# Kernel tuning notes

Measured on AMD Instinct MI355X. Metric: run time of the kernel, lower is better.

## Reference

```python
import jax, jax.numpy as jnp
import numpy as np

TEMP = 1.0
EULER_GAMMA = 0.5772156649015329
BIG = 1.0e9


def setup_inputs() -> dict:
    key = jax.random.key(0)
    k = jax.random.split(key, 8)
    B, N, D, H = 32, 1024, 1024, 512  # batch, seq, d_model, hidden_size//2
    queries = jax.random.normal(k[0], (B, N, D), jnp.float32)
    queries_mask = jnp.ones((B, N), dtype=bool)
    W1 = jax.random.normal(k[1], (D, H), jnp.float32) * 0.02
    b1 = jnp.zeros((H,), jnp.float32)
    W2 = jax.random.normal(k[2], (H, 1), jnp.float32) * 0.02
    b2 = jnp.zeros((1,), jnp.float32)
    uniform_noise = jax.random.uniform(k[3], (B, N, 1), jnp.float32, 0.0, 1e-5)
    gumbel_noise = jax.random.gumbel(k[4], (B, N, 1), jnp.float32)
    return {"queries": queries, "queries_mask": queries_mask, "W1": W1, "b1": b1,
            "W2": W2, "b2": b2, "uniform_noise": uniform_noise,
            "gumbel_noise": gumbel_noise, "action_refinement": 1}


def reference(queries, queries_mask, W1, b1, W2, b2, uniform_noise, gumbel_noise, action_refinement):
    B, N, D = queries.shape
    # block0: Dense(H, relu) -> Dense(1); then softplus clamp + log + tiny uniform noise
    h = jax.nn.relu(jnp.einsum('bnd,dh->bnh', queries, W1) + b1)
    acts = jnp.einsum('bnh,ho->bno', h, W2) + b2                      # [B,N,1]
    acts = jnp.log(jnp.maximum(jax.nn.softplus(acts), 1e-5)) + uniform_noise
    acts = jnp.repeat(acts, action_refinement, axis=0)                # [BR,N,1]
    vmask = jnp.repeat(queries_mask[:, None, :].astype(jnp.float32), action_refinement, axis=0)  # [BR,1,N]
    n_valid = jnp.sum(vmask, axis=-1)                                 # [BR,1]
    mask_n1 = jnp.transpose(vmask, (0, 2, 1))                         # [BR,N,1]
    sqz_mask = mask_n1[..., 0]                                        # [BR,N]
    masked_acts = jnp.where(mask_n1 > 0, acts, -1e6)                  # [BR,N,1]
    perturb = masked_acts + gumbel_noise                              # [BR,N,1]
    # deterministic NeuralSort
    s = (jnp.exp(perturb) * mask_n1)[..., 0]                          # [BR,N]
    A = jnp.abs(s[:, :, None] - s[:, None, :])                        # [BR,N,N]
    Bmat = jnp.sum(A, axis=-1, keepdims=True)                         # A @ (1 1^T): row sums broadcast
    scaling = (N + 1 - 2 * (jnp.arange(N) + 1)).astype(jnp.float32)   # [N]
    C = s[:, :, None] * scaling[None, None, :]                        # [BR,N,N]
    P_hat = jnp.transpose(C - Bmat, (0, 2, 1)) - (1.0 - vmask) * BIG  # [BR,N,N]
    # greedy argmax permutation extraction (find_permu), vectorized over batch
    BR = P_hat.shape[0]
    def step(flag, row):                                              # row: [BR,N]
        tmp = row - flag * BIG
        idx = jnp.argmax(tmp, axis=-1)
        flag = jnp.maximum(flag, jax.nn.one_hot(idx, N, dtype=flag.dtype))
        return flag, idx
    _, idxs = jax.lax.scan(step, jnp.zeros((BR, N), jnp.float32), jnp.transpose(P_hat, (1, 0, 2)))
    chosen = jnp.transpose(idxs).astype(jnp.int32)                    # [BR,N]
    chosen = jnp.concatenate([jnp.zeros((BR, 1), jnp.int32), chosen[:, :-1]], axis=-1)
    id_permu = jnp.arange(N, dtype=jnp.int32)[None, :]
    permu = jnp.where(sqz_mask > 0, chosen, id_permu)                 # [BR,N]
    sample_permu = jax.nn.one_hot(permu, N, axis=-1, dtype=jnp.float32)
    # Plackett-Luce log-likelihood of sampled permutation
    exp_actis = jnp.exp(jnp.take_along_axis(masked_acts[..., 0], permu, axis=-1))
    rev_cumsum = jnp.cumsum(exp_actis[:, ::-1], axis=-1)[:, ::-1]
    eps = 1e-20
    log_nom = (jnp.log(exp_actis + eps) - jnp.log(rev_cumsum + eps)) * sqz_mask
    log_nom = jnp.sum(log_nom, axis=-1, keepdims=True)                # [BR,1]
    log_norm = jnp.zeros_like(log_nom)
    # KL term
    sqz_acts = acts[..., 0]
    kl1 = n_valid * (np.log(TEMP) - 1.0 + EULER_GAMMA * (1.0 / TEMP - 1.0))
    s1 = (1.0 / TEMP) * jnp.sum(sqz_acts * sqz_mask, axis=-1).reshape(-1, 1)
    s2 = jnp.sum(jnp.exp(-1.0 / TEMP * jnp.maximum(sqz_acts * sqz_mask, -20.0 * TEMP)), axis=-1).reshape(-1, 1) - (jnp.float32(N) - n_valid)
    kl = kl1 + s1 + s2 * jnp.exp(jax.lax.lgamma(jnp.float32(1.0 + 1.0 / TEMP)))
    return sample_permu, masked_acts[..., 0], kl, log_nom, log_norm
```

## Files before the change

### kernel.cpp

```cpp
#include <hip/hip_runtime.h>
#include <math.h>

#define BB 32
#define NN 1024
#define DD 1024
#define HH 512

#define OUT0_OFF 0
#define OUT1_OFF (BB * NN * NN)
#define OUT2_OFF (OUT1_OFF + BB * NN)
#define OUT3_OFF (OUT2_OFF + BB)
#define OUT4_OFF (OUT3_OFF + BB)

#define WS_ACTS 0
#define WS_W1T  131072
#define WS_RANK 1179648

typedef __attribute__((ext_vector_type(8))) short short8;
typedef __attribute__((ext_vector_type(4))) float floatx4;
typedef __attribute__((ext_vector_type(4))) unsigned int uintx4;

__device__ inline unsigned int cvtpk(float a, float b) {
    unsigned int r;
    asm("v_cvt_pk_bf16_f32 %0, %1, %2" : "=v"(r) : "v"(a), "v"(b));
    return r;
}

__global__ __launch_bounds__(64) void w1t_kernel(const float* __restrict__ W1,
                                                 unsigned short* __restrict__ Bfrag)
{
    const int s  = blockIdx.x;
    const int tn = blockIdx.y;
    const int l  = threadIdx.x;
    const int c  = l & 15, qd = l >> 4;
    const int n  = tn * 16 + c;
    float v[8];
    #pragma unroll
    for (int e = 0; e < 8; ++e)
        v[e] = W1[(size_t)(s * 32 + qd * 8 + e) * HH + n];
    uintx4 u;
    u.x = cvtpk(v[0], v[1]);
    u.y = cvtpk(v[2], v[3]);
    u.z = cvtpk(v[4], v[5]);
    u.w = cvtpk(v[6], v[7]);
    *(uintx4*)(Bfrag + ((size_t)(s * 32 + tn) * 64 + l) * 8) = u;
}

#define MT 64

__global__ __launch_bounds__(256, 2) void gemm_acts_kernel(
    const float* __restrict__ q, const unsigned short* __restrict__ Bfrag,
    const float* __restrict__ b1, const float* __restrict__ W2,
    const float* __restrict__ b2, const float* __restrict__ unoise,
    float* __restrict__ acts_ws, float* __restrict__ out1)
{
    __shared__ float red[MT][4];

    const int tid  = threadIdx.x;
    const int w    = tid >> 6;
    const int lane = tid & 63;
    const int c    = lane & 15;
    const int qd   = lane >> 4;
    const int m0   = blockIdx.x * MT;

    floatx4 acc[8][4];
    #pragma unroll
    for (int tn = 0; tn < 8; ++tn)
        #pragma unroll
        for (int tm = 0; tm < 4; ++tm)
            acc[tn][tm] = (floatx4){0.f, 0.f, 0.f, 0.f};

    const float* aptr[4];
    #pragma unroll
    for (int tm = 0; tm < 4; ++tm)
        aptr[tm] = q + (size_t)(m0 + tm * 16 + c) * DD + qd * 8;

    const short8* bp = (const short8*)Bfrag;
    const int bbase = w * 8 * 64 + lane;

    #pragma unroll 2
    for (int s = 0; s < 32; ++s) {
        short8 af[4];
        #pragma unroll
        for (int tm = 0; tm < 4; ++tm) {
            float4 v0 = *(const float4*)(aptr[tm] + s * 32);
            float4 v1 = *(const float4*)(aptr[tm] + s * 32 + 4);
            uintx4 u;
            u.x = cvtpk(v0.x, v0.y);
            u.y = cvtpk(v0.z, v0.w);
            u.z = cvtpk(v1.x, v1.y);
            u.w = cvtpk(v1.z, v1.w);
            af[tm] = __builtin_bit_cast(short8, u);
        }
        #pragma unroll
        for (int tn = 0; tn < 8; ++tn) {
            short8 bf = bp[(size_t)s * 32 * 64 + bbase + tn * 64];
            #pragma unroll
            for (int tm = 0; tm < 4; ++tm)
                acc[tn][tm] = __builtin_amdgcn_mfma_f32_16x16x32_bf16(
                    af[tm], bf, acc[tn][tm], 0, 0, 0);
        }
    }

    float b1v[8], w2v[8];
    #pragma unroll
    for (int tn = 0; tn < 8; ++tn) {
        int col = w * 128 + tn * 16 + c;
        b1v[tn] = b1[col];
        w2v[tn] = W2[col];
    }
    #pragma unroll
    for (int tm = 0; tm < 4; ++tm) {
        #pragma unroll
        for (int r = 0; r < 4; ++r) {
            float p = 0.f;
            #pragma unroll
            for (int tn = 0; tn < 8; ++tn) {
                float v = acc[tn][tm][r] + b1v[tn];
                p = fmaf(fmaxf(v, 0.f), w2v[tn], p);
            }
            p += __shfl_xor(p, 1);
            p += __shfl_xor(p, 2);
            p += __shfl_xor(p, 4);
            p += __shfl_xor(p, 8);
            if (c == 0) red[tm * 16 + qd * 4 + r][w] = p;
        }
    }
    __syncthreads();
    if (tid < MT) {
        float raw = red[tid][0] + red[tid][1] + red[tid][2] + red[tid][3] + b2[0];
        float sp = fmaxf(raw, 0.f) + log1pf(expf(-fabsf(raw)));
        int row = m0 + tid;
        float av = logf(fmaxf(sp, 1e-5f)) + unoise[row];
        acts_ws[row] = av;
        out1[row]    = av;
    }
}

__global__ __launch_bounds__(256) void zero_kernel(float4* __restrict__ p, int n4)
{
    int idx = blockIdx.x * blockDim.x + threadIdx.x;
    int stride = gridDim.x * blockDim.x;
    float4 z = make_float4(0.f, 0.f, 0.f, 0.f);
    for (int i = idx; i < n4; i += stride) p[i] = z;
}

__global__ __launch_bounds__(256) void rank_kernel(
    const float* __restrict__ acts_ws, const float* __restrict__ gumbel,
    int* __restrict__ rank)
{
    __shared__ float P[NN];
    const int b = blockIdx.x >> 2;
    const int chunk = blockIdx.x & 3;
    const int tid = threadIdx.x;
    #pragma unroll
    for (int r = 0; r < 4; ++r) {
        int j = r * 256 + tid;
        P[j] = acts_ws[b * NN + j] + gumbel[b * NN + j];
    }
    __syncthreads();
    const int i = chunk * 256 + tid;
    const float pert = P[i];
    int cnt = 0;
    const float4* P4 = (const float4*)P;
    for (int j4 = 0; j4 < NN / 4; ++j4) {
        float4 pv = P4[j4];
        int j = j4 * 4;
        cnt += (pv.x > pert) || (pv.x == pert && j + 0 < i);
        cnt += (pv.y > pert) || (pv.y == pert && j + 1 < i);
        cnt += (pv.z > pert) || (pv.z == pert && j + 2 < i);
        cnt += (pv.w > pert) || (pv.w == pert && j + 3 < i);
    }
    rank[b * NN + i] = cnt;
}

__global__ __launch_bounds__(1024) void permu_stats_kernel(
    const float* __restrict__ acts_ws, const int* __restrict__ rank,
    float* __restrict__ out0, float* __restrict__ out2,
    float* __restrict__ out3, float* __restrict__ out4)
{
    __shared__ float A[NN];
    __shared__ int   IDX[NN];
    __shared__ float WT[16];
    __shared__ float WSUF[17];
    __shared__ float P0[16], P1[16], P2[16];

    const int b = blockIdx.x;
    const int i = threadIdx.x;
    const int lane = i & 63;
    const int w = i >> 6;

    float a = acts_ws[b * NN + i];
    A[i] = a;
    IDX[rank[b * NN + i]] = i;
    __syncthreads();

    int perm = (i == 0) ? 0 : IDX[i - 1];
    out0[((size_t)b * NN + i) * NN + perm] = 1.0f;

    float e = expf(A[perm]);
    float s = e;
    #pragma unroll
    for (int off = 1; off < 64; off <<= 1) {
        float v = __shfl_down(s, off);
        if (lane + off < 64) s += v;
    }
    if (lane == 0) WT[w] = s;
    __syncthreads();
    if (w == 0) {
        float t = (lane < 16) ? WT[lane] : 0.f;
        #pragma unroll
        for (int off = 1; off < 16; off <<= 1) {
            float v = __shfl_down(t, off);
            if (lane + off < 16) t += v;
        }
        if (lane < 16) WSUF[lane] = t;
        if (lane == 0) WSUF[16] = 0.f;
    }
    __syncthreads();

    float S = s + WSUF[w + 1];
    float term = logf(e + 1e-20f) - logf(S + 1e-20f);

    float r0 = term, r1 = a, r2 = expf(-fmaxf(a, -20.f));
    #pragma unroll
    for (int off = 1; off < 64; off <<= 1) {
        r0 += __shfl_xor(r0, off);
        r1 += __shfl_xor(r1, off);
        r2 += __shfl_xor(r2, off);
    }
    if (lane == 0) { P0[w] = r0; P1[w] = r1; P2[w] = r2; }
    __syncthreads();
    if (i == 0) {
        float t0 = 0.f, t1 = 0.f, t2 = 0.f;
        #pragma unroll
        for (int k = 0; k < 16; ++k) { t0 += P0[k]; t1 += P1[k]; t2 += P2[k]; }
        out3[b] = t0;
        out2[b] = -(float)NN + t1 + t2;
        out4[b] = 0.f;
    }
}

extern "C" void kernel_launch(void* const* d_in, const int* in_sizes, int n_in,
                              void* d_out, int out_size, void* d_ws, size_t ws_size,
                              hipStream_t stream)
{
    const float* q      = (const float*)d_in[0];
    const float* W1     = (const float*)d_in[2];
    const float* b1     = (const float*)d_in[3];
    const float* W2     = (const float*)d_in[4];
    const float* b2     = (const float*)d_in[5];
    const float* unoise = (const float*)d_in[6];
    const float* gumbel = (const float*)d_in[7];

    float* out  = (float*)d_out;
    char*  ws   = (char*)d_ws;
    float*          acts  = (float*)(ws + WS_ACTS);
    unsigned short* Bfrag = (unsigned short*)(ws + WS_W1T);
    int*            rank  = (int*)(ws + WS_RANK);

    w1t_kernel<<<dim3(32, 32), 64, 0, stream>>>(W1, Bfrag);
    gemm_acts_kernel<<<(BB * NN) / MT, 256, 0, stream>>>(q, Bfrag, b1, W2, b2,
                                                         unoise, acts,
                                                         out + OUT1_OFF);
    zero_kernel<<<8192, 256, 0, stream>>>((float4*)(out + OUT0_OFF),
                                          (BB * NN * NN) / 4);
    rank_kernel<<<BB * 4, 256, 0, stream>>>(acts, gumbel, rank);
    permu_stats_kernel<<<BB, 1024, 0, stream>>>(acts, rank,
                                                out + OUT0_OFF, out + OUT2_OFF,
                                                out + OUT3_OFF, out + OUT4_OFF);
}
```

Measured before the change: 345.3 us.

## Stage bf16 A tile in swizzled LDS and split GEMM across 8 waves

The GEMM kernel now loads the whole 64x1024 fp32 query tile once, converts it to bf16 with a software round-to-nearest-even routine, and stores it in LDS (128 KB) using an XOR swizzle. The block grows to 512 threads, with 8 waves arranged 2x4, so each wave handles 32 rows instead of 64 and keeps half as many accumulators. The intent is to cut register pressure and raise the number of waves per block, replacing strided global A loads inside the K loop with LDS reads. The trade-off is a large LDS footprint that probably allows only one block per CU, plus a fully serial global-load phase before any MFMA work starts, and the inline cvt_pk asm is swapped for the slower software rounding.

```diff
diff --git a/kernel.cpp b/kernel.cpp
--- a/kernel.cpp
+++ b/kernel.cpp
@@ -20,10 +20,9 @@
 typedef __attribute__((ext_vector_type(4))) float floatx4;
 typedef __attribute__((ext_vector_type(4))) unsigned int uintx4;
 
-__device__ inline unsigned int cvtpk(float a, float b) {
-    unsigned int r;
-    asm("v_cvt_pk_bf16_f32 %0, %1, %2" : "=v"(r) : "v"(a), "v"(b));
-    return r;
+__device__ inline unsigned int f2bf(float x) {
+    unsigned int u = __builtin_bit_cast(unsigned int, x);
+    return (u + 0x7FFFu + ((u >> 16) & 1u)) >> 16;
 }
 
 __global__ __launch_bounds__(64) void w1t_kernel(const float* __restrict__ W1,
@@ -39,78 +38,99 @@
     for (int e = 0; e < 8; ++e)
         v[e] = W1[(size_t)(s * 32 + qd * 8 + e) * HH + n];
     uintx4 u;
-    u.x = cvtpk(v[0], v[1]);
-    u.y = cvtpk(v[2], v[3]);
-    u.z = cvtpk(v[4], v[5]);
-    u.w = cvtpk(v[6], v[7]);
+    u.x = f2bf(v[0]) | (f2bf(v[1]) << 16);
+    u.y = f2bf(v[2]) | (f2bf(v[3]) << 16);
+    u.z = f2bf(v[4]) | (f2bf(v[5]) << 16);
+    u.w = f2bf(v[6]) | (f2bf(v[7]) << 16);
     *(uintx4*)(Bfrag + ((size_t)(s * 32 + tn) * 64 + l) * 8) = u;
 }
 
 #define MT 64
 
-__global__ __launch_bounds__(256, 2) void gemm_acts_kernel(
+__global__ __launch_bounds__(512, 2) void gemm_acts_kernel(
     const float* __restrict__ q, const unsigned short* __restrict__ Bfrag,
     const float* __restrict__ b1, const float* __restrict__ W2,
     const float* __restrict__ b2, const float* __restrict__ unoise,
     float* __restrict__ acts_ws, float* __restrict__ out1)
 {
-    __shared__ float red[MT][4];
+    __shared__ short As[MT * DD];
 
     const int tid  = threadIdx.x;
     const int w    = tid >> 6;
     const int lane = tid & 63;
     const int c    = lane & 15;
     const int qd   = lane >> 4;
+    const int wr   = (w >> 2) * 32;
+    const int wc   = (w & 3) * 128;
     const int m0   = blockIdx.x * MT;
 
-    floatx4 acc[8][4];
+    floatx4 acc[8][2];
     #pragma unroll
     for (int tn = 0; tn < 8; ++tn)
         #pragma unroll
-        for (int tm = 0; tm < 4; ++tm)
+        for (int tm = 0; tm < 2; ++tm)
             acc[tn][tm] = (floatx4){0.f, 0.f, 0.f, 0.f};
 
-    const float* aptr[4];
-    #pragma unroll
-    for (int tm = 0; tm < 4; ++tm)
-        aptr[tm] = q + (size_t)(m0 + tm * 16 + c) * DD + qd * 8;
+    {
+        const int ar = tid >> 3;
+        const int ub = tid & 7;
+        const int s7 = ar & 7;
+        const float* arp = q + (size_t)(m0 + ar) * DD;
+        char* adst = (char*)As + ar * 2048;
+        #pragma unroll
+        for (int i = 0; i < 16; ++i) {
+            int u = ub + i * 8;
+            int g = u ^ s7;
+            float4 v0 = *(const float4*)(arp + g * 8);
+            float4 v1 = *(const float4*)(arp + g * 8 + 4);
+            uint4 pk;
+            pk.x = f2bf(v0.x) | (f2bf(v0.y) << 16);
+            pk.y = f2bf(v0.z) | (f2bf(v0.w) << 16);
+            pk.z = f2bf(v1.x) | (f2bf(v1.y) << 16);
+            pk.w = f2bf(v1.z) | (f2bf(v1.w) << 16);
+            *(uint4*)(adst + u * 16) = pk;
+        }
+    }
+    __syncthreads();
+
+    const char* asb = (const char*)As;
+    int arow_b[2];
+    #pragma unroll
+    for (int tm = 0; tm < 2; ++tm)
+        arow_b[tm] = (wr + tm * 16 + c) * 2048;
+    const int axor = (c & 7);
 
     const short8* bp = (const short8*)Bfrag;
-    const int bbase = w * 8 * 64 + lane;
+    const int bbase = ((w & 3) * 8) * 64 + lane;
 
     #pragma unroll 2
     for (int s = 0; s < 32; ++s) {
-        short8 af[4];
-        #pragma unroll
-        for (int tm = 0; tm < 4; ++tm) {
-            float4 v0 = *(const float4*)(aptr[tm] + s * 32);
-            float4 v1 = *(const float4*)(aptr[tm] + s * 32 + 4);
-            uintx4 u;
-            u.x = cvtpk(v0.x, v0.y);
-            u.y = cvtpk(v0.z, v0.w);
-            u.z = cvtpk(v1.x, v1.y);
-            u.w = cvtpk(v1.z, v1.w);
-            af[tm] = __builtin_bit_cast(short8, u);
-        }
+        const int au = ((s * 4 + qd) ^ axor) * 16;
+        short8 af[2];
+        #pragma unroll
+        for (int tm = 0; tm < 2; ++tm)
+            af[tm] = *(const short8*)(asb + arow_b[tm] + au);
         #pragma unroll
         for (int tn = 0; tn < 8; ++tn) {
-            short8 bf = bp[(size_t)s * 32 * 64 + bbase + tn * 64];
+            short8 bf = bp[(size_t)s * 2048 + bbase + tn * 64];
             #pragma unroll
-            for (int tm = 0; tm < 4; ++tm)
+            for (int tm = 0; tm < 2; ++tm)
                 acc[tn][tm] = __builtin_amdgcn_mfma_f32_16x16x32_bf16(
                     af[tm], bf, acc[tn][tm], 0, 0, 0);
         }
     }
 
+    float (*red)[4] = (float (*)[4])As;
     float b1v[8], w2v[8];
     #pragma unroll
     for (int tn = 0; tn < 8; ++tn) {
-        int col = w * 128 + tn * 16 + c;
+        int col = wc + tn * 16 + c;
         b1v[tn] = b1[col];
         w2v[tn] = W2[col];
     }
-    #pragma unroll
-    for (int tm = 0; tm < 4; ++tm) {
+    __syncthreads();
+    #pragma unroll
+    for (int tm = 0; tm < 2; ++tm) {
         #pragma unroll
         for (int r = 0; r < 4; ++r) {
             float p = 0.f;
@@ -123,7 +143,7 @@
             p += __shfl_xor(p, 2);
             p += __shfl_xor(p, 4);
             p += __shfl_xor(p, 8);
-            if (c == 0) red[tm * 16 + qd * 4 + r][w] = p;
+            if (c == 0) red[wr + tm * 16 + qd * 4 + r][w & 3] = p;
         }
     }
     __syncthreads();
@@ -260,7 +280,7 @@
     int*            rank  = (int*)(ws + WS_RANK);
 
     w1t_kernel<<<dim3(32, 32), 64, 0, stream>>>(W1, Bfrag);
-    gemm_acts_kernel<<<(BB * NN) / MT, 256, 0, stream>>>(q, Bfrag, b1, W2, b2,
+    gemm_acts_kernel<<<(BB * NN) / MT, 512, 0, stream>>>(q, Bfrag, b1, W2, b2,
                                                          unoise, acts,
                                                          out + OUT1_OFF);
     zero_kernel<<<8192, 256, 0, stream>>>((float4*)(out + OUT0_OFF),
```

Result: slower. 366.2 us (+6.1%).
